# Optimization experiments

Measured on AMD Instinct MI355X. Metric: run time of the kernel, lower is better.

## Reference

```python
import jax, jax.numpy as jnp
import numpy as np

EMB = 1024
HEADS = 16
HEAD_DIM = EMB // HEADS
CTX = 2048
BATCH = 4
LN_EPS = 1e-5


def layer_norm(x, g, b):
    mu = jnp.mean(x, axis=-1, keepdims=True)
    var = jnp.mean(jnp.square(x - mu), axis=-1, keepdims=True)
    return (x - mu) * jax.lax.rsqrt(var + LN_EPS) * g + b


def setup_inputs() -> dict:
    key = jax.random.key(0)
    ks = jax.random.split(key, 12)
    s_in = 1.0 / np.sqrt(EMB)
    s_ff = 1.0 / np.sqrt(4 * EMB)
    return {
        "x": jax.random.normal(ks[0], (BATCH, CTX, EMB), jnp.float32),
        # per-head Q/K/V projections, no bias (matches Head linears)
        "wq": jax.random.normal(ks[1], (HEADS, EMB, HEAD_DIM), jnp.float32) * s_in,
        "wk": jax.random.normal(ks[2], (HEADS, EMB, HEAD_DIM), jnp.float32) * s_in,
        "wv": jax.random.normal(ks[3], (HEADS, EMB, HEAD_DIM), jnp.float32) * s_in,
        "w_proj": jax.random.normal(ks[4], (EMB, EMB), jnp.float32) * s_in,
        "b_proj": jnp.zeros((EMB,), jnp.float32),
        "w1": jax.random.normal(ks[5], (EMB, 4 * EMB), jnp.float32) * s_in,
        "b1": jnp.zeros((4 * EMB,), jnp.float32),
        "w2": jax.random.normal(ks[6], (4 * EMB, EMB), jnp.float32) * s_ff,
        "b2": jnp.zeros((EMB,), jnp.float32),
        "ln1_g": jnp.ones((EMB,), jnp.float32),
        "ln1_b": jnp.zeros((EMB,), jnp.float32),
        "ln2_g": jnp.ones((EMB,), jnp.float32),
        "ln2_b": jnp.zeros((EMB,), jnp.float32),
    }


def reference(x, wq, wk, wv, w_proj, b_proj, w1, b1, w2, b2, ln1_g, ln1_b, ln2_g, ln2_b):
    B, T, C = x.shape
    # --- attention branch (pre-LN) ---
    h = layer_norm(x, ln1_g, ln1_b)
    q = jnp.einsum('btc,hcd->bhtd', h, wq)
    k = jnp.einsum('btc,hcd->bhtd', h, wk)
    v = jnp.einsum('btc,hcd->bhtd', h, wv)
    scale = 1.0 / np.sqrt(HEAD_DIM)
    scores = jnp.einsum('bhtd,bhsd->bhts', q, k) * scale  # [B,H,T,T]
    causal = jnp.tril(jnp.ones((T, T), dtype=bool))
    scores = jnp.where(causal, scores, -jnp.inf)
    attn = jax.nn.softmax(scores, axis=-1)
    out = jnp.einsum('bhts,bhsd->bhtd', attn, v)
    out = out.transpose(0, 2, 1, 3).reshape(B, T, C)  # concat heads
    out = out @ w_proj.T + b_proj if False else jnp.einsum('btc,cd->btd', out, w_proj) + b_proj
    x = x + out
    # --- FFN branch (pre-LN) ---
    h2 = layer_norm(x, ln2_g, ln2_b)
    ff = jax.nn.relu(jnp.einsum('btc,cf->btf', h2, w1) + b1)
    ff = jnp.einsum('btf,fc->btc', ff, w2) + b2
    return x + ff
```

## Files before the change

kernel.cpp:

```cpp
#include <hip/hip_runtime.h>


#define DEVI __device__ __forceinline__

typedef float  f32x4  __attribute__((ext_vector_type(4)));
typedef float  f32x16 __attribute__((ext_vector_type(16)));
typedef __bf16 bf16x8 __attribute__((ext_vector_type(8)));
typedef short  s16x8  __attribute__((ext_vector_type(8)));
typedef unsigned int u32x4 __attribute__((ext_vector_type(4)));
typedef unsigned short u16;

DEVI u16 f2bf(float f) {
    return __builtin_bit_cast(u16, (__bf16)f);
}

DEVI unsigned pk2(float lo, float hi2) {
    return (unsigned)f2bf(lo) | ((unsigned)f2bf(hi2) << 16);
}

DEVI void gload_lds16(const void* g, void* l) {
    __builtin_amdgcn_global_load_lds(
        (__attribute__((address_space(1))) void*)(g),
        (__attribute__((address_space(3))) void*)(l), 16, 0, 0);
}

DEVI f32x4 mfma16(s16x8 a, s16x8 b, f32x4 c) {
    return __builtin_amdgcn_mfma_f32_16x16x32_bf16(
        __builtin_bit_cast(bf16x8, a), __builtin_bit_cast(bf16x8, b), c, 0, 0, 0);
}

DEVI f32x16 mfma32(s16x8 a, s16x8 b, f32x16 c) {
    return __builtin_amdgcn_mfma_f32_32x32x16_bf16(
        __builtin_bit_cast(bf16x8, a), __builtin_bit_cast(bf16x8, b), c, 0, 0, 0);
}

__global__ __launch_bounds__(256) void transpose_cvt(
    const float* __restrict__ src, u16* __restrict__ dst,
    int K, int N, long srcStride, long dstStride)
{
    __shared__ float t[64][65];
    src += (long)blockIdx.z * srcStride;
    dst += (long)blockIdx.z * dstStride;
    int k0 = blockIdx.x * 64, n0 = blockIdx.y * 64;
    int tx = threadIdx.x & 63, ty = threadIdx.x >> 6;
#pragma unroll
    for (int i = 0; i < 16; ++i) {
        int r = ty * 16 + i;
        t[r][tx] = src[(long)(k0 + r) * N + n0 + tx];
    }
    __syncthreads();
#pragma unroll
    for (int i = 0; i < 16; ++i) {
        int r = ty * 16 + i;
        dst[(long)(n0 + r) * K + k0 + tx] = f2bf(t[tx][r]);
    }
}

__global__ __launch_bounds__(256) void ln_bf16(
    const float* __restrict__ x, const float* __restrict__ g,
    const float* __restrict__ b, u16* __restrict__ out)
{
    int row = blockIdx.x, tid = threadIdx.x;
    const float4 v = ((const float4*)(x + (long)row * 1024))[tid];
    float s = v.x + v.y + v.z + v.w;
    float q = v.x * v.x + v.y * v.y + v.z * v.z + v.w * v.w;
#pragma unroll
    for (int m = 1; m < 64; m <<= 1) { s += __shfl_xor(s, m); q += __shfl_xor(q, m); }
    __shared__ float red[8];
    int lane = tid & 63, w = tid >> 6;
    if (lane == 0) { red[w] = s; red[w + 4] = q; }
    __syncthreads();
    s = red[0] + red[1] + red[2] + red[3];
    q = red[4] + red[5] + red[6] + red[7];
    float mu  = s * (1.0f / 1024.0f);
    float var = q * (1.0f / 1024.0f) - mu * mu;
    float rs  = rsqrtf(var + 1e-5f);
    float4 gv = ((const float4*)g)[tid];
    float4 bv = ((const float4*)b)[tid];
    ushort4 o;
    o.x = f2bf((v.x - mu) * rs * gv.x + bv.x);
    o.y = f2bf((v.y - mu) * rs * gv.y + bv.y);
    o.z = f2bf((v.z - mu) * rs * gv.z + bv.z);
    o.w = f2bf((v.w - mu) * rs * gv.w + bv.w);
    ((ushort4*)(out + (long)row * 1024))[tid] = o;
}

template <int EPI>
__global__ __launch_bounds__(256, 3) void gemm_bt(
    const u16* __restrict__ A, const u16* __restrict__ Bt,
    int M, int N, int K,
    float* __restrict__ outF, u16* __restrict__ outB,
    const float* __restrict__ bias, const float* __restrict__ resid,
    u16* __restrict__ qd, u16* __restrict__ kd, u16* __restrict__ vd)
{
    __shared__ alignas(16) u16 As[128 * 32];
    __shared__ alignas(16) u16 Bs[128 * 32];
    int tid = threadIdx.x;
    int lane = tid & 63, w = tid >> 6;
    int wm = w & 1, wn = w >> 1;
    int l15 = lane & 15, l4 = lane >> 4;
    long m0 = (long)blockIdx.x * 128, n0 = (long)blockIdx.y * 128;
    const u16* Ag = A + m0 * K;
    const u16* Bg = Bt + n0 * K;
    int scol = (lane & 3) * 8;
    int srow0 = (w * 2 + 0) * 16 + (lane >> 2);
    int srow1 = (w * 2 + 1) * 16 + (lane >> 2);

    f32x4 acc[4][4] = {};

    for (int kt = 0; kt < K; kt += 32) {
        gload_lds16(Ag + (long)srow0 * K + kt + scol, &As[(w * 2 + 0) * 512]);
        gload_lds16(Ag + (long)srow1 * K + kt + scol, &As[(w * 2 + 1) * 512]);
        gload_lds16(Bg + (long)srow0 * K + kt + scol, &Bs[(w * 2 + 0) * 512]);
        gload_lds16(Bg + (long)srow1 * K + kt + scol, &Bs[(w * 2 + 1) * 512]);
        __syncthreads();
        s16x8 a[4], b[4];
#pragma unroll
        for (int m = 0; m < 4; ++m)
            a[m] = *(const s16x8*)&As[(wm * 64 + m * 16 + l15) * 32 + l4 * 8];
#pragma unroll
        for (int n = 0; n < 4; ++n)
            b[n] = *(const s16x8*)&Bs[(wn * 64 + n * 16 + l15) * 32 + l4 * 8];
#pragma unroll
        for (int m = 0; m < 4; ++m)
#pragma unroll
            for (int n = 0; n < 4; ++n)
                acc[m][n] = mfma16(a[m], b[n], acc[m][n]);
        __syncthreads();
    }

    long mbase = m0 + wm * 64;
    long nbase = n0 + wn * 64;
#pragma unroll
    for (int m = 0; m < 4; ++m)
#pragma unroll
        for (int n = 0; n < 4; ++n)
#pragma unroll
            for (int r = 0; r < 4; ++r) {
                long row = mbase + m * 16 + l4 * 4 + r;
                long col = nbase + n * 16 + l15;
                float val = acc[m][n][r];
                if constexpr (EPI == 0) {
                    int c = (int)col;
                    int which = c >> 10, hh = (c >> 6) & 15, dd = c & 63;
                    int bb = (int)(row >> 11), tt = (int)(row & 2047);
                    if (which == 2) {
                        vd[((long)(bb * 16 + hh) * 64 + dd) * 2048 + tt] = f2bf(val);
                    } else {
                        u16* dst = which == 0 ? qd : kd;
                        dst[((long)(bb * 16 + hh) * 2048 + tt) * 64 + dd] = f2bf(val);
                    }
                } else if constexpr (EPI == 1) {
                    outF[row * N + col] = val + bias[col] + resid[row * N + col];
                } else {
                    float t2 = val + bias[col];
                    outB[row * N + col] = f2bf(t2 > 0.f ? t2 : 0.f);
                }
            }
}

__global__ __launch_bounds__(256, 4) void attn_kernel(
    const u16* __restrict__ Q, const u16* __restrict__ K,
    const u16* __restrict__ Vt, u16* __restrict__ O)
{
    constexpr int PAD = 72;
    constexpr float SC2 = 0.125f * 1.44269504088896f;
    constexpr float THR = 11.5416f;
    __shared__ alignas(16) u16 Ks[2][64 * PAD];
    __shared__ alignas(16) u16 Vts[2][64 * PAD];
    __shared__ alignas(16) float xbuf[4][32];
    int tid = threadIdx.x, lane = tid & 63, w = tid >> 6;
    int l31 = lane & 31, hi = lane >> 5;
    bool h = (hi != 0);
    int qp = blockIdx.x, hh = blockIdx.y, bb = blockIdx.z;
    const long hbase = ((long)(bb * 16 + hh)) * 2048 * 64;

    int srow[2], scol8[2];
#pragma unroll
    for (int i = 0; i < 2; ++i) {
        int c = tid + 256 * i;
        srow[i] = c >> 3;
        scol8[i] = (c & 7) * 8;
    }

#pragma unroll 1
    for (int ph = 0; ph < 2; ++ph) {
        int qt = ph == 0 ? qp : 15 - qp;
        int q0w = qt * 128 + w * 32;
        int nt = 2 * qt + 2;
        int qv = q0w + l31;

        s16x8 bq[4];
#pragma unroll
        for (int c = 0; c < 4; ++c)
            bq[c] = *(const s16x8*)&Q[hbase + (long)(q0w + l31) * 64 + c * 16 + hi * 8];

        f32x16 o0 = {}, o1 = {};
        float mrow = -1e30f, lrow = 0.f;

        s16x8 kr[2], vr[2];
        {
            const u16* Kg = K + hbase;
            const u16* Vg = Vt + hbase;
#pragma unroll
            for (int i = 0; i < 2; ++i) {
                s16x8 k0 = *(const s16x8*)&Kg[srow[i] * 64 + scol8[i]];
                s16x8 v0 = *(const s16x8*)&Vg[(long)srow[i] * 2048 + scol8[i]];
                *(s16x8*)&Ks[0][srow[i] * PAD + scol8[i]]  = k0;
                *(s16x8*)&Vts[0][srow[i] * PAD + scol8[i]] = v0;
            }
            if (nt > 1) {
                const u16* Kg1 = K + hbase + 64 * 64;
                const u16* Vg1 = Vt + hbase + 64;
#pragma unroll
                for (int i = 0; i < 2; ++i) {
                    kr[i] = *(const s16x8*)&Kg1[srow[i] * 64 + scol8[i]];
                    vr[i] = *(const s16x8*)&Vg1[(long)srow[i] * 2048 + scol8[i]];
                }
            }
        }
        __syncthreads();

#pragma unroll 1
        for (int kt = 0; kt < nt; ++kt) {
            int cur = kt & 1;
            if (kt + 1 < nt) {
#pragma unroll
                for (int i = 0; i < 2; ++i) {
                    *(s16x8*)&Ks[cur ^ 1][srow[i] * PAD + scol8[i]]  = kr[i];
                    *(s16x8*)&Vts[cur ^ 1][srow[i] * PAD + scol8[i]] = vr[i];
                }
            }
            if (kt + 2 < nt) {
                const u16* Kg = K + hbase + (long)(kt + 2) * 64 * 64;
                const u16* Vg = Vt + hbase + (long)(kt + 2) * 64;
#pragma unroll
                for (int i = 0; i < 2; ++i) {
                    kr[i] = *(const s16x8*)&Kg[srow[i] * 64 + scol8[i]];
                    vr[i] = *(const s16x8*)&Vg[(long)srow[i] * 2048 + scol8[i]];
                }
            }

#pragma unroll
            for (int k2 = 0; k2 < 2; ++k2) {
                int kbase = kt * 64 + k2 * 32;
                if (kbase <= q0w + 31) {
                    f32x16 s = {};
                    __builtin_amdgcn_s_setprio(1);
#pragma unroll
                    for (int c = 0; c < 4; ++c) {
                        s16x8 ak = *(const s16x8*)&Ks[cur][(k2 * 32 + l31) * PAD + c * 16 + hi * 8];
                        s = mfma32(ak, bq[c], s);
                    }
                    __builtin_amdgcn_s_setprio(0);

                    int khi = kbase + 4 * hi;
                    if (kbase + 31 > q0w) {
#pragma unroll
                        for (int r = 0; r < 16; ++r) {
                            int kg = khi + ((r & 3) + 8 * (r >> 2));
                            float sv = s[r] * SC2;
                            s[r] = (kg > qv) ? -1e30f : sv;
                        }
                    } else {
#pragma unroll
                        for (int r = 0; r < 16; ++r) s[r] *= SC2;
                    }

                    float t8[8], t4[4], t2[2];
#pragma unroll
                    for (int r = 0; r < 8; ++r) t8[r] = fmaxf(s[r], s[r + 8]);
#pragma unroll
                    for (int r = 0; r < 4; ++r) t4[r] = fmaxf(t8[r], t8[r + 4]);
                    t2[0] = fmaxf(t4[0], t4[2]); t2[1] = fmaxf(t4[1], t4[3]);
                    float pm = fmaxf(t2[0], t2[1]);
                    pm = fmaxf(pm, __shfl_xor(pm, 32));

                    int allok = __all(pm - mrow <= THR);
                    float ef = 1.f;
                    if (!allok) {
                        float mn = fmaxf(mrow, pm);
                        ef = exp2f(mrow - mn);
                        mrow = mn;
                    }
                    float a8[8], a4[4];
#pragma unroll
                    for (int r = 0; r < 16; ++r) s[r] = exp2f(s[r] - mrow);
#pragma unroll
                    for (int r = 0; r < 8; ++r) a8[r] = s[r] + s[r + 8];
#pragma unroll
                    for (int r = 0; r < 4; ++r) a4[r] = a8[r] + a8[r + 4];
                    float rsum = (a4[0] + a4[1]) + (a4[2] + a4[3]);
                    rsum += __shfl_xor(rsum, 32);

                    if (!allok) {
                        lrow = lrow * ef + rsum;
                        xbuf[w][l31] = ef;
#pragma unroll
                        for (int rr = 0; rr < 4; ++rr) {
                            f32x4 efv = *(const f32x4*)&xbuf[w][rr * 8 + hi * 4];
#pragma unroll
                            for (int j = 0; j < 4; ++j) {
                                o0[rr * 4 + j] *= efv[j];
                                o1[rr * 4 + j] *= efv[j];
                            }
                        }
                    } else {
                        lrow += rsum;
                    }

                    unsigned c0 = pk2(s[0],  s[1]),  c1 = pk2(s[2],  s[3]);
                    unsigned c2 = pk2(s[4],  s[5]),  c3 = pk2(s[6],  s[7]);
                    unsigned c4 = pk2(s[8],  s[9]),  c5 = pk2(s[10], s[11]);
                    unsigned c6 = pk2(s[12], s[13]), c7 = pk2(s[14], s[15]);
                    unsigned x0 = __shfl_xor((int)c0, 32), x1 = __shfl_xor((int)c1, 32);
                    unsigned x2 = __shfl_xor((int)c2, 32), x3 = __shfl_xor((int)c3, 32);
                    unsigned x4 = __shfl_xor((int)c4, 32), x5 = __shfl_xor((int)c5, 32);
                    unsigned x6 = __shfl_xor((int)c6, 32), x7 = __shfl_xor((int)c7, 32);
                    u32x4 w0 = { h ? x2 : c0, h ? x3 : c1, h ? c2 : x0, h ? c3 : x1 };
                    u32x4 w1 = { h ? x6 : c4, h ? x7 : c5, h ? c6 : x4, h ? c7 : x5 };
                    s16x8 pa0 = __builtin_bit_cast(s16x8, w0);
                    s16x8 pa1 = __builtin_bit_cast(s16x8, w1);

                    __builtin_amdgcn_s_setprio(1);
#pragma unroll
                    for (int ks = 0; ks < 2; ++ks) {
                        s16x8 pa = ks ? pa1 : pa0;
                        s16x8 bv0 = *(const s16x8*)&Vts[cur][(l31) * PAD + k2 * 32 + ks * 16 + hi * 8];
                        s16x8 bv1 = *(const s16x8*)&Vts[cur][(32 + l31) * PAD + k2 * 32 + ks * 16 + hi * 8];
                        o0 = mfma32(pa, bv0, o0);
                        o1 = mfma32(pa, bv1, o1);
                    }
                    __builtin_amdgcn_s_setprio(0);
                }
            }
            __syncthreads();
        }

        float il = 1.0f / lrow;
        xbuf[w][l31] = il;
        f32x4 ilv[4];
#pragma unroll
        for (int rr = 0; rr < 4; ++rr)
            ilv[rr] = *(const f32x4*)&xbuf[w][rr * 8 + hi * 4];
#pragma unroll
        for (int r = 0; r < 16; ++r) {
            int t = q0w + ((r & 3) + 8 * (r >> 2)) + 4 * hi;
            float sc = ilv[r >> 2][r & 3];
            long rbase = ((long)(bb * 2048 + t)) * 1024 + hh * 64;
            O[rbase + l31]      = f2bf(o0[r] * sc);
            O[rbase + 32 + l31] = f2bf(o1[r] * sc);
        }
        __syncthreads();
    }
}

extern "C" void kernel_launch(void* const* d_in, const int* in_sizes, int n_in,
                              void* d_out, int out_size, void* d_ws, size_t ws_size,
                              hipStream_t stream)
{
    const float* x      = (const float*)d_in[0];
    const float* wq     = (const float*)d_in[1];
    const float* wk     = (const float*)d_in[2];
    const float* wv     = (const float*)d_in[3];
    const float* w_proj = (const float*)d_in[4];
    const float* b_proj = (const float*)d_in[5];
    const float* w1     = (const float*)d_in[6];
    const float* b1     = (const float*)d_in[7];
    const float* w2     = (const float*)d_in[8];
    const float* b2     = (const float*)d_in[9];
    const float* ln1_g  = (const float*)d_in[10];
    const float* ln1_b  = (const float*)d_in[11];
    const float* ln2_g  = (const float*)d_in[12];
    const float* ln2_b  = (const float*)d_in[13];

    char* ws = (char*)d_ws;
    u16*   WQKVt = (u16*)(ws + 0);
    u16*   WPt   = (u16*)(ws + 6291456);
    u16*   W1t   = (u16*)(ws + 8388608);
    u16*   W2t   = (u16*)(ws + 16777216);
    u16*   H     = (u16*)(ws + 25165824);
    u16*   Qb    = (u16*)(ws + 41943040);
    u16*   Kb    = (u16*)(ws + 58720256);
    u16*   Vb    = (u16*)(ws + 75497472);
    u16*   Ob    = (u16*)(ws + 92274688);
    u16*   FF    = (u16*)(ws + 41943040);
    float* X1    = (float*)(ws + 109051904);
    float* out   = (float*)d_out;

    transpose_cvt<<<dim3(16, 1, 16), 256, 0, stream>>>(wq, WQKVt,           1024, 64, 65536, 65536);
    transpose_cvt<<<dim3(16, 1, 16), 256, 0, stream>>>(wk, WQKVt + 1048576, 1024, 64, 65536, 65536);
    transpose_cvt<<<dim3(16, 1, 16), 256, 0, stream>>>(wv, WQKVt + 2097152, 1024, 64, 65536, 65536);
    transpose_cvt<<<dim3(16, 16, 1), 256, 0, stream>>>(w_proj, WPt, 1024, 1024, 0, 0);
    transpose_cvt<<<dim3(16, 64, 1), 256, 0, stream>>>(w1, W1t, 1024, 4096, 0, 0);
    transpose_cvt<<<dim3(64, 16, 1), 256, 0, stream>>>(w2, W2t, 4096, 1024, 0, 0);

    ln_bf16<<<8192, 256, 0, stream>>>(x, ln1_g, ln1_b, H);

    gemm_bt<0><<<dim3(64, 24), 256, 0, stream>>>(H, WQKVt, 8192, 3072, 1024,
        nullptr, nullptr, nullptr, nullptr, Qb, Kb, Vb);

    attn_kernel<<<dim3(8, 16, 4), 256, 0, stream>>>(Qb, Kb, Vb, Ob);

    gemm_bt<1><<<dim3(64, 8), 256, 0, stream>>>(Ob, WPt, 8192, 1024, 1024,
        X1, nullptr, b_proj, x, nullptr, nullptr, nullptr);

    ln_bf16<<<8192, 256, 0, stream>>>(X1, ln2_g, ln2_b, H);

    gemm_bt<2><<<dim3(64, 32), 256, 0, stream>>>(H, W1t, 8192, 4096, 1024,
        nullptr, FF, b1, nullptr, nullptr, nullptr, nullptr);

    gemm_bt<1><<<dim3(64, 8), 256, 0, stream>>>(FF, W2t, 8192, 1024, 4096,
        out, nullptr, b2, X1, nullptr, nullptr, nullptr);
}
```

Before: 427.7 us.

## Add 256x256-tile double-buffered GEMM for QKV and FFN1 projections

Adds a new 512-thread GEMM kernel with 256x256 output tiles, a K-step of 64, XOR-swizzled LDS loaded directly from global memory, and double buffering. The next tile's loads overlap with MFMA phases that are separated by barriers and run under raised wave priority. The block index is also remapped so neighbouring workgroups share operand tiles in cache. The QKV and FFN1 GEMMs now use this kernel to get more data reuse per LDS load and better latency hiding. The costs are much higher register and LDS use per block and fewer blocks per wave.

Result: slower. 460.8 us (+7.7%).

```diff
diff --git a/kernel.cpp b/kernel.cpp
--- a/kernel.cpp
+++ b/kernel.cpp
@@ -83,6 +83,157 @@
     o.z = f2bf((v.z - mu) * rs * gv.z + bv.z);
     o.w = f2bf((v.w - mu) * rs * gv.w + bv.w);
     ((ushort4*)(out + (long)row * 1024))[tid] = o;
+}
+
+template <int EPI>
+__global__ __launch_bounds__(512, 2) void gemm256(
+    const u16* __restrict__ A, const u16* __restrict__ Bt,
+    int M, int N, int K,
+    u16* __restrict__ outB, const float* __restrict__ bias,
+    u16* __restrict__ qd, u16* __restrict__ kd, u16* __restrict__ vd)
+{
+    __shared__ alignas(16) u16 lds[2][2][16384];
+    int tid = threadIdx.x, lane = tid & 63, w = tid >> 6;
+    int l15 = lane & 15, l4 = lane >> 4;
+    int wm = w >> 2, wn = w & 3;
+
+    int gx = gridDim.x;
+    int nwg = gx * gridDim.y;
+    int bid = blockIdx.y * gx + blockIdx.x;
+    int swz = (bid & 7) * (nwg >> 3) + (bid >> 3);
+    int bx = swz % gx, by = swz / gx;
+    long m0 = (long)bx * 256, n0 = (long)by * 256;
+
+    int srow8 = lane >> 3;
+    int sc = ((lane & 7) ^ srow8) * 8;
+    const u16* Ags = A + (m0 + w * 8 + srow8) * (long)K + sc;
+    const u16* Bgs = Bt + (n0 + w * 8 + srow8) * (long)K + sc;
+    int ldsw = w * 512;
+
+    int rc0 = (l4 * 8) ^ ((l15 & 7) * 8);
+    int rc1 = (32 + l4 * 8) ^ ((l15 & 7) * 8);
+
+    f32x4 acc[8][4] = {};
+
+#pragma unroll
+    for (int i = 0; i < 4; ++i) {
+        gload_lds16(Ags + (long)i * 64 * K, &lds[0][0][i * 4096 + ldsw]);
+        gload_lds16(Bgs + (long)i * 64 * K, &lds[0][1][i * 4096 + ldsw]);
+    }
+    asm volatile("s_waitcnt vmcnt(0)" ::: "memory");
+    __builtin_amdgcn_s_barrier();
+
+    int NT = K >> 6;
+#pragma unroll 1
+    for (int t = 0; t < NT; ++t) {
+        int cur = t & 1;
+        const u16* As_ = &lds[cur][0][0];
+        const u16* Bs_ = &lds[cur][1][0];
+
+        s16x8 a0[4], b0[4];
+#pragma unroll
+        for (int i = 0; i < 4; ++i)
+            a0[i] = *(const s16x8*)&As_[(wm * 128 + i * 16 + l15) * 64 + rc0];
+#pragma unroll
+        for (int n = 0; n < 4; ++n)
+            b0[n] = *(const s16x8*)&Bs_[(wn * 64 + n * 16 + l15) * 64 + rc0];
+        if (t + 1 < NT) {
+            long kt = (long)(t + 1) * 64;
+#pragma unroll
+            for (int i = 0; i < 4; ++i) {
+                gload_lds16(Ags + (long)i * 64 * K + kt, &lds[cur ^ 1][0][i * 4096 + ldsw]);
+                gload_lds16(Bgs + (long)i * 64 * K + kt, &lds[cur ^ 1][1][i * 4096 + ldsw]);
+            }
+        }
+        __builtin_amdgcn_s_barrier();
+        asm volatile("s_waitcnt lgkmcnt(0)" ::: "memory");
+        __builtin_amdgcn_sched_barrier(0);
+        __builtin_amdgcn_s_setprio(1);
+#pragma unroll
+        for (int mi = 0; mi < 4; ++mi)
+#pragma unroll
+            for (int n = 0; n < 4; ++n)
+                acc[mi][n] = mfma16(a0[mi], b0[n], acc[mi][n]);
+        __builtin_amdgcn_s_setprio(0);
+        __builtin_amdgcn_s_barrier();
+
+        s16x8 a1[4];
+#pragma unroll
+        for (int i = 0; i < 4; ++i)
+            a1[i] = *(const s16x8*)&As_[(wm * 128 + 64 + i * 16 + l15) * 64 + rc0];
+        __builtin_amdgcn_s_barrier();
+        asm volatile("s_waitcnt lgkmcnt(0)" ::: "memory");
+        __builtin_amdgcn_sched_barrier(0);
+        __builtin_amdgcn_s_setprio(1);
+#pragma unroll
+        for (int mi = 0; mi < 4; ++mi)
+#pragma unroll
+            for (int n = 0; n < 4; ++n)
+                acc[4 + mi][n] = mfma16(a1[mi], b0[n], acc[4 + mi][n]);
+        __builtin_amdgcn_s_setprio(0);
+        __builtin_amdgcn_s_barrier();
+
+        s16x8 a2[4], b1v[4];
+#pragma unroll
+        for (int i = 0; i < 4; ++i)
+            a2[i] = *(const s16x8*)&As_[(wm * 128 + i * 16 + l15) * 64 + rc1];
+#pragma unroll
+        for (int n = 0; n < 4; ++n)
+            b1v[n] = *(const s16x8*)&Bs_[(wn * 64 + n * 16 + l15) * 64 + rc1];
+        __builtin_amdgcn_s_barrier();
+        asm volatile("s_waitcnt lgkmcnt(0)" ::: "memory");
+        __builtin_amdgcn_sched_barrier(0);
+        __builtin_amdgcn_s_setprio(1);
+#pragma unroll
+        for (int mi = 0; mi < 4; ++mi)
+#pragma unroll
+            for (int n = 0; n < 4; ++n)
+                acc[mi][n] = mfma16(a2[mi], b1v[n], acc[mi][n]);
+        __builtin_amdgcn_s_setprio(0);
+        __builtin_amdgcn_s_barrier();
+
+        s16x8 a3[4];
+#pragma unroll
+        for (int i = 0; i < 4; ++i)
+            a3[i] = *(const s16x8*)&As_[(wm * 128 + 64 + i * 16 + l15) * 64 + rc1];
+        __builtin_amdgcn_s_barrier();
+        asm volatile("s_waitcnt lgkmcnt(0)" ::: "memory");
+        __builtin_amdgcn_sched_barrier(0);
+        __builtin_amdgcn_s_setprio(1);
+#pragma unroll
+        for (int mi = 0; mi < 4; ++mi)
+#pragma unroll
+            for (int n = 0; n < 4; ++n)
+                acc[4 + mi][n] = mfma16(a3[mi], b1v[n], acc[4 + mi][n]);
+        __builtin_amdgcn_s_setprio(0);
+        asm volatile("s_waitcnt vmcnt(0)" ::: "memory");
+        __builtin_amdgcn_s_barrier();
+    }
+
+#pragma unroll
+    for (int mf = 0; mf < 8; ++mf)
+#pragma unroll
+        for (int n = 0; n < 4; ++n)
+#pragma unroll
+            for (int r = 0; r < 4; ++r) {
+                long row = m0 + wm * 128 + mf * 16 + l4 * 4 + r;
+                long col = n0 + wn * 64 + n * 16 + l15;
+                float val = acc[mf][n][r];
+                if constexpr (EPI == 0) {
+                    int c = (int)col;
+                    int which = c >> 10, hh = (c >> 6) & 15, dd = c & 63;
+                    int bb = (int)(row >> 11), tt = (int)(row & 2047);
+                    if (which == 2) {
+                        vd[((long)(bb * 16 + hh) * 64 + dd) * 2048 + tt] = f2bf(val);
+                    } else {
+                        u16* dst = which == 0 ? qd : kd;
+                        dst[((long)(bb * 16 + hh) * 2048 + tt) * 64 + dd] = f2bf(val);
+                    }
+                } else {
+                    float t2 = val + bias[col];
+                    outB[row * N + col] = f2bf(t2 > 0.f ? t2 : 0.f);
+                }
+            }
 }
 
 template <int EPI>
@@ -140,21 +291,8 @@
                 long row = mbase + m * 16 + l4 * 4 + r;
                 long col = nbase + n * 16 + l15;
                 float val = acc[m][n][r];
-                if constexpr (EPI == 0) {
-                    int c = (int)col;
-                    int which = c >> 10, hh = (c >> 6) & 15, dd = c & 63;
-                    int bb = (int)(row >> 11), tt = (int)(row & 2047);
-                    if (which == 2) {
-                        vd[((long)(bb * 16 + hh) * 64 + dd) * 2048 + tt] = f2bf(val);
-                    } else {
-                        u16* dst = which == 0 ? qd : kd;
-                        dst[((long)(bb * 16 + hh) * 2048 + tt) * 64 + dd] = f2bf(val);
-                    }
-                } else if constexpr (EPI == 1) {
+                if constexpr (EPI == 1) {
                     outF[row * N + col] = val + bias[col] + resid[row * N + col];
-                } else {
-                    float t2 = val + bias[col];
-                    outB[row * N + col] = f2bf(t2 > 0.f ? t2 : 0.f);
                 }
             }
 }
@@ -397,8 +535,8 @@
 
     ln_bf16<<<8192, 256, 0, stream>>>(x, ln1_g, ln1_b, H);
 
-    gemm_bt<0><<<dim3(64, 24), 256, 0, stream>>>(H, WQKVt, 8192, 3072, 1024,
-        nullptr, nullptr, nullptr, nullptr, Qb, Kb, Vb);
+    gemm256<0><<<dim3(32, 12), 512, 0, stream>>>(H, WQKVt, 8192, 3072, 1024,
+        nullptr, nullptr, Qb, Kb, Vb);
 
     attn_kernel<<<dim3(8, 16, 4), 256, 0, stream>>>(Qb, Kb, Vb, Ob);
 
@@ -407,8 +545,8 @@
 
     ln_bf16<<<8192, 256, 0, stream>>>(X1, ln2_g, ln2_b, H);
 
-    gemm_bt<2><<<dim3(64, 32), 256, 0, stream>>>(H, W1t, 8192, 4096, 1024,
-        nullptr, FF, b1, nullptr, nullptr, nullptr, nullptr);
+    gemm256<2><<<dim3(32, 16), 512, 0, stream>>>(H, W1t, 8192, 4096, 1024,
+        FF, b1, nullptr, nullptr, nullptr);
 
     gemm_bt<1><<<dim3(64, 8), 256, 0, stream>>>(FF, W2t, 8192, 1024, 4096,
         out, nullptr, b2, X1, nullptr, nullptr, nullptr);
```

## Add 256x256-tile pipelined GEMM for QKV and FFN1 projections

Applied to the files above, without the earlier changes.

Introduces a 512-thread GEMM kernel with 256x256 output tiles, a 4-slot LDS ring with two tiles of prefetch via direct global-to-LDS loads, XOR-swizzled LDS layout, and block-index swizzling for L2 locality. It replaces the 128x128 kernel for the QKV and first FFN GEMMs to raise data reuse per LDS load and overlap loads with MFMA work. Costs include larger LDS use, 128 accumulator registers per thread, and fewer workgroups (384/512), which may leave CUs idle or create wave-quantization tails.

Measured after the change: 453.5 us. 1.06x slower.

```diff
diff --git a/kernel.cpp b/kernel.cpp
--- a/kernel.cpp
+++ b/kernel.cpp
@@ -83,6 +83,131 @@
     o.z = f2bf((v.z - mu) * rs * gv.z + bv.z);
     o.w = f2bf((v.w - mu) * rs * gv.w + bv.w);
     ((ushort4*)(out + (long)row * 1024))[tid] = o;
+}
+
+template <int EPI>
+__global__ __launch_bounds__(512, 2) void gemm256(
+    const u16* __restrict__ A, const u16* __restrict__ Bt,
+    int M, int N, int K,
+    u16* __restrict__ outB, const float* __restrict__ bias,
+    u16* __restrict__ qd, u16* __restrict__ kd, u16* __restrict__ vd)
+{
+    __shared__ alignas(16) u16 lds[4][2][8192];
+    int tid = threadIdx.x, lane = tid & 63, w = tid >> 6;
+    int l15 = lane & 15, l4 = lane >> 4;
+    int wm = w >> 2, wn = w & 3;
+
+    int gx = gridDim.x;
+    int nwg = gx * gridDim.y;
+    int bid = blockIdx.y * gx + blockIdx.x;
+    int swz = (bid & 7) * (nwg >> 3) + (bid >> 3);
+    int bx = swz % gx, by = swz / gx;
+    long m0 = (long)bx * 256, n0 = (long)by * 256;
+
+    long soff0, soff1; int ldso0, ldso1;
+    {
+        int cI0 = w * 64 + lane;
+        int r0 = cI0 >> 2, p0 = cI0 & 3;
+        soff0 = (long)r0 * K + (p0 ^ ((r0 >> 1) & 3)) * 8;
+        ldso0 = w * 512;
+        int cI1 = 512 + cI0;
+        int r1 = cI1 >> 2, p1 = cI1 & 3;
+        soff1 = (long)r1 * K + (p1 ^ ((r1 >> 1) & 3)) * 8;
+        ldso1 = 4096 + w * 512;
+    }
+    const u16* Ag = A + m0 * K;
+    const u16* Bg = Bt + n0 * K;
+
+#define STAGE(tt) do {                                                  \
+        int _b = (tt) & 3;                                              \
+        long _kt = (long)(tt) * 32;                                     \
+        gload_lds16(Ag + soff0 + _kt, &lds[_b][0][ldso0]);              \
+        gload_lds16(Bg + soff0 + _kt, &lds[_b][1][ldso0]);              \
+        gload_lds16(Ag + soff1 + _kt, &lds[_b][0][ldso1]);              \
+        gload_lds16(Bg + soff1 + _kt, &lds[_b][1][ldso1]);              \
+    } while (0)
+
+    int rc = (l4 ^ ((l15 >> 1) & 3)) * 8;
+
+    f32x4 acc[8][4] = {};
+
+    STAGE(0);
+    STAGE(1);
+    asm volatile("s_waitcnt vmcnt(4)" ::: "memory");
+    __builtin_amdgcn_s_barrier();
+
+    int NT = K >> 5;
+#pragma unroll 1
+    for (int t = 0; t < NT; ++t) {
+        int cb = t & 3;
+        const u16* As_ = &lds[cb][0][0];
+        const u16* Bs_ = &lds[cb][1][0];
+
+        if (t + 2 < NT) STAGE(t + 2);
+
+        s16x8 a[8], b[4];
+#pragma unroll
+        for (int i = 0; i < 4; ++i)
+            a[i] = *(const s16x8*)&As_[(wm * 128 + i * 16 + l15) * 32 + rc];
+#pragma unroll
+        for (int n = 0; n < 4; ++n)
+            b[n] = *(const s16x8*)&Bs_[(wn * 64 + n * 16 + l15) * 32 + rc];
+#pragma unroll
+        for (int i = 0; i < 4; ++i)
+            a[4 + i] = *(const s16x8*)&As_[(wm * 128 + 64 + i * 16 + l15) * 32 + rc];
+
+        asm volatile("s_waitcnt lgkmcnt(4)" ::: "memory");
+        __builtin_amdgcn_sched_barrier(0);
+        __builtin_amdgcn_s_setprio(1);
+#pragma unroll
+        for (int mi = 0; mi < 4; ++mi)
+#pragma unroll
+            for (int n = 0; n < 4; ++n)
+                acc[mi][n] = mfma16(a[mi], b[n], acc[mi][n]);
+        __builtin_amdgcn_s_setprio(0);
+
+        asm volatile("s_waitcnt lgkmcnt(0)" ::: "memory");
+        __builtin_amdgcn_sched_barrier(0);
+        __builtin_amdgcn_s_setprio(1);
+#pragma unroll
+        for (int mi = 0; mi < 4; ++mi)
+#pragma unroll
+            for (int n = 0; n < 4; ++n)
+                acc[4 + mi][n] = mfma16(a[4 + mi], b[n], acc[4 + mi][n]);
+        __builtin_amdgcn_s_setprio(0);
+
+        if (t + 2 < NT)
+            asm volatile("s_waitcnt vmcnt(4)" ::: "memory");
+        else
+            asm volatile("s_waitcnt vmcnt(0)" ::: "memory");
+        __builtin_amdgcn_s_barrier();
+    }
+#undef STAGE
+
+#pragma unroll
+    for (int mf = 0; mf < 8; ++mf)
+#pragma unroll
+        for (int n = 0; n < 4; ++n)
+#pragma unroll
+            for (int r = 0; r < 4; ++r) {
+                long row = m0 + wm * 128 + mf * 16 + l4 * 4 + r;
+                long col = n0 + wn * 64 + n * 16 + l15;
+                float val = acc[mf][n][r];
+                if constexpr (EPI == 0) {
+                    int c = (int)col;
+                    int which = c >> 10, hh = (c >> 6) & 15, dd = c & 63;
+                    int bb = (int)(row >> 11), tt = (int)(row & 2047);
+                    if (which == 2) {
+                        vd[((long)(bb * 16 + hh) * 64 + dd) * 2048 + tt] = f2bf(val);
+                    } else {
+                        u16* dst = which == 0 ? qd : kd;
+                        dst[((long)(bb * 16 + hh) * 2048 + tt) * 64 + dd] = f2bf(val);
+                    }
+                } else {
+                    float t2 = val + bias[col];
+                    outB[row * N + col] = f2bf(t2 > 0.f ? t2 : 0.f);
+                }
+            }
 }
 
 template <int EPI>
@@ -140,21 +265,8 @@
                 long row = mbase + m * 16 + l4 * 4 + r;
                 long col = nbase + n * 16 + l15;
                 float val = acc[m][n][r];
-                if constexpr (EPI == 0) {
-                    int c = (int)col;
-                    int which = c >> 10, hh = (c >> 6) & 15, dd = c & 63;
-                    int bb = (int)(row >> 11), tt = (int)(row & 2047);
-                    if (which == 2) {
-                        vd[((long)(bb * 16 + hh) * 64 + dd) * 2048 + tt] = f2bf(val);
-                    } else {
-                        u16* dst = which == 0 ? qd : kd;
-                        dst[((long)(bb * 16 + hh) * 2048 + tt) * 64 + dd] = f2bf(val);
-                    }
-                } else if constexpr (EPI == 1) {
+                if constexpr (EPI == 1) {
                     outF[row * N + col] = val + bias[col] + resid[row * N + col];
-                } else {
-                    float t2 = val + bias[col];
-                    outB[row * N + col] = f2bf(t2 > 0.f ? t2 : 0.f);
                 }
             }
 }
@@ -397,8 +509,8 @@
 
     ln_bf16<<<8192, 256, 0, stream>>>(x, ln1_g, ln1_b, H);
 
-    gemm_bt<0><<<dim3(64, 24), 256, 0, stream>>>(H, WQKVt, 8192, 3072, 1024,
-        nullptr, nullptr, nullptr, nullptr, Qb, Kb, Vb);
+    gemm256<0><<<dim3(32, 12), 512, 0, stream>>>(H, WQKVt, 8192, 3072, 1024,
+        nullptr, nullptr, Qb, Kb, Vb);
 
     attn_kernel<<<dim3(8, 16, 4), 256, 0, stream>>>(Qb, Kb, Vb, Ob);
 
@@ -407,8 +519,8 @@
 
     ln_bf16<<<8192, 256, 0, stream>>>(X1, ln2_g, ln2_b, H);
 
-    gemm_bt<2><<<dim3(64, 32), 256, 0, stream>>>(H, W1t, 8192, 4096, 1024,
-        nullptr, FF, b1, nullptr, nullptr, nullptr, nullptr);
+    gemm256<2><<<dim3(32, 16), 512, 0, stream>>>(H, W1t, 8192, 4096, 1024,
+        FF, b1, nullptr, nullptr, nullptr);
 
     gemm_bt<1><<<dim3(64, 8), 256, 0, stream>>>(FF, W2t, 8192, 1024, 4096,
         out, nullptr, b2, X1, nullptr, nullptr, nullptr);
```

## Drop paired causal tiles per block and process 64-key softmax tiles at once

Applied to the files above, without the earlier changes.

The attention kernel no longer pairs a light and heavy query tile in one block; each block now handles a single 128-row query tile, and the grid doubles to 1024 blocks. The inner loop also computes both 32-key halves of a 64-key tile before one combined online-softmax update, halving max/sum reductions and rescale checks. This risks load imbalance across blocks, since causal tiles vary in cost, and raises register pressure from holding two score tiles.

New measurement: 507.0 us. +18.5%, slower.

```diff
diff --git a/kernel.cpp b/kernel.cpp
--- a/kernel.cpp
+++ b/kernel.cpp
@@ -172,7 +172,7 @@
     int tid = threadIdx.x, lane = tid & 63, w = tid >> 6;
     int l31 = lane & 31, hi = lane >> 5;
     bool h = (hi != 0);
-    int qp = blockIdx.x, hh = blockIdx.y, bb = blockIdx.z;
+    int qt = blockIdx.x, hh = blockIdx.y, bb = blockIdx.z;
     const long hbase = ((long)(bb * 16 + hh)) * 2048 * 64;
 
     int srow[2], scol8[2];
@@ -183,175 +183,209 @@
         scol8[i] = (c & 7) * 8;
     }
 
+    int q0w = qt * 128 + w * 32;
+    int nt = 2 * qt + 2;
+    int qv = q0w + l31;
+
+    s16x8 bq[4];
+#pragma unroll
+    for (int c = 0; c < 4; ++c)
+        bq[c] = *(const s16x8*)&Q[hbase + (long)(q0w + l31) * 64 + c * 16 + hi * 8];
+
+    f32x16 o0 = {}, o1 = {};
+    float mrow = -1e30f, lrow = 0.f;
+
+    s16x8 kr[2], vr[2];
+    {
+        const u16* Kg = K + hbase;
+        const u16* Vg = Vt + hbase;
+#pragma unroll
+        for (int i = 0; i < 2; ++i) {
+            s16x8 k0 = *(const s16x8*)&Kg[srow[i] * 64 + scol8[i]];
+            s16x8 v0 = *(const s16x8*)&Vg[(long)srow[i] * 2048 + scol8[i]];
+            *(s16x8*)&Ks[0][srow[i] * PAD + scol8[i]]  = k0;
+            *(s16x8*)&Vts[0][srow[i] * PAD + scol8[i]] = v0;
+        }
+        if (nt > 1) {
+            const u16* Kg1 = K + hbase + 64 * 64;
+            const u16* Vg1 = Vt + hbase + 64;
+#pragma unroll
+            for (int i = 0; i < 2; ++i) {
+                kr[i] = *(const s16x8*)&Kg1[srow[i] * 64 + scol8[i]];
+                vr[i] = *(const s16x8*)&Vg1[(long)srow[i] * 2048 + scol8[i]];
+            }
+        }
+    }
+    __syncthreads();
+
 #pragma unroll 1
-    for (int ph = 0; ph < 2; ++ph) {
-        int qt = ph == 0 ? qp : 15 - qp;
-        int q0w = qt * 128 + w * 32;
-        int nt = 2 * qt + 2;
-        int qv = q0w + l31;
-
-        s16x8 bq[4];
-#pragma unroll
-        for (int c = 0; c < 4; ++c)
-            bq[c] = *(const s16x8*)&Q[hbase + (long)(q0w + l31) * 64 + c * 16 + hi * 8];
-
-        f32x16 o0 = {}, o1 = {};
-        float mrow = -1e30f, lrow = 0.f;
-
-        s16x8 kr[2], vr[2];
-        {
-            const u16* Kg = K + hbase;
-            const u16* Vg = Vt + hbase;
+    for (int kt = 0; kt < nt; ++kt) {
+        int cur = kt & 1;
+        if (kt + 1 < nt) {
 #pragma unroll
             for (int i = 0; i < 2; ++i) {
-                s16x8 k0 = *(const s16x8*)&Kg[srow[i] * 64 + scol8[i]];
-                s16x8 v0 = *(const s16x8*)&Vg[(long)srow[i] * 2048 + scol8[i]];
-                *(s16x8*)&Ks[0][srow[i] * PAD + scol8[i]]  = k0;
-                *(s16x8*)&Vts[0][srow[i] * PAD + scol8[i]] = v0;
-            }
-            if (nt > 1) {
-                const u16* Kg1 = K + hbase + 64 * 64;
-                const u16* Vg1 = Vt + hbase + 64;
-#pragma unroll
-                for (int i = 0; i < 2; ++i) {
-                    kr[i] = *(const s16x8*)&Kg1[srow[i] * 64 + scol8[i]];
-                    vr[i] = *(const s16x8*)&Vg1[(long)srow[i] * 2048 + scol8[i]];
-                }
-            }
+                *(s16x8*)&Ks[cur ^ 1][srow[i] * PAD + scol8[i]]  = kr[i];
+                *(s16x8*)&Vts[cur ^ 1][srow[i] * PAD + scol8[i]] = vr[i];
+            }
+        }
+        if (kt + 2 < nt) {
+            const u16* Kg = K + hbase + (long)(kt + 2) * 64 * 64;
+            const u16* Vg = Vt + hbase + (long)(kt + 2) * 64;
+#pragma unroll
+            for (int i = 0; i < 2; ++i) {
+                kr[i] = *(const s16x8*)&Kg[srow[i] * 64 + scol8[i]];
+                vr[i] = *(const s16x8*)&Vg[(long)srow[i] * 2048 + scol8[i]];
+            }
+        }
+
+        int kb0 = kt * 64;
+        if (kb0 <= q0w + 31) {
+            bool live1 = (kb0 + 32 <= q0w + 31);
+
+            f32x16 s0 = {}, s1;
+            __builtin_amdgcn_s_setprio(1);
+#pragma unroll
+            for (int c = 0; c < 4; ++c) {
+                s16x8 ak = *(const s16x8*)&Ks[cur][(l31) * PAD + c * 16 + hi * 8];
+                s0 = mfma32(ak, bq[c], s0);
+            }
+            __builtin_amdgcn_s_setprio(0);
+            if (live1) {
+                f32x16 z = {};
+                __builtin_amdgcn_s_setprio(1);
+#pragma unroll
+                for (int c = 0; c < 4; ++c) {
+                    s16x8 ak = *(const s16x8*)&Ks[cur][(32 + l31) * PAD + c * 16 + hi * 8];
+                    z = mfma32(ak, bq[c], z);
+                }
+                __builtin_amdgcn_s_setprio(0);
+                s1 = z;
+            } else {
+#pragma unroll
+                for (int r = 0; r < 16; ++r) s1[r] = -1e30f;
+            }
+
+            int khi0 = kb0 + 4 * hi;
+            if (kb0 + 31 > q0w) {
+#pragma unroll
+                for (int r = 0; r < 16; ++r) {
+                    int kg = khi0 + ((r & 3) + 8 * (r >> 2));
+                    s0[r] = (kg > qv) ? -1e30f : s0[r] * SC2;
+                }
+            } else {
+#pragma unroll
+                for (int r = 0; r < 16; ++r) s0[r] *= SC2;
+            }
+            if (live1) {
+                int kb1 = kb0 + 32;
+                int khi1 = kb1 + 4 * hi;
+                if (kb1 + 31 > q0w) {
+#pragma unroll
+                    for (int r = 0; r < 16; ++r) {
+                        int kg = khi1 + ((r & 3) + 8 * (r >> 2));
+                        s1[r] = (kg > qv) ? -1e30f : s1[r] * SC2;
+                    }
+                } else {
+#pragma unroll
+                    for (int r = 0; r < 16; ++r) s1[r] *= SC2;
+                }
+            }
+
+            float m16[16];
+#pragma unroll
+            for (int r = 0; r < 16; ++r) m16[r] = fmaxf(s0[r], s1[r]);
+            float m8[8], m4[4];
+#pragma unroll
+            for (int r = 0; r < 8; ++r) m8[r] = fmaxf(m16[r], m16[r + 8]);
+#pragma unroll
+            for (int r = 0; r < 4; ++r) m4[r] = fmaxf(m8[r], m8[r + 4]);
+            float pm = fmaxf(fmaxf(m4[0], m4[1]), fmaxf(m4[2], m4[3]));
+            pm = fmaxf(pm, __shfl_xor(pm, 32));
+
+            int allok = __all(pm - mrow <= THR);
+            float ef = 1.f;
+            if (!allok) {
+                float mn = fmaxf(mrow, pm);
+                ef = exp2f(mrow - mn);
+                mrow = mn;
+            }
+#pragma unroll
+            for (int r = 0; r < 16; ++r) s0[r] = exp2f(s0[r] - mrow);
+#pragma unroll
+            for (int r = 0; r < 16; ++r) s1[r] = exp2f(s1[r] - mrow);
+            float a16[16];
+#pragma unroll
+            for (int r = 0; r < 16; ++r) a16[r] = s0[r] + s1[r];
+            float a8[8], a4[4];
+#pragma unroll
+            for (int r = 0; r < 8; ++r) a8[r] = a16[r] + a16[r + 8];
+#pragma unroll
+            for (int r = 0; r < 4; ++r) a4[r] = a8[r] + a8[r + 4];
+            float rsum = (a4[0] + a4[1]) + (a4[2] + a4[3]);
+            rsum += __shfl_xor(rsum, 32);
+
+            if (!allok) {
+                lrow = lrow * ef + rsum;
+                xbuf[w][l31] = ef;
+#pragma unroll
+                for (int rr = 0; rr < 4; ++rr) {
+                    f32x4 efv = *(const f32x4*)&xbuf[w][rr * 8 + hi * 4];
+#pragma unroll
+                    for (int j = 0; j < 4; ++j) {
+                        o0[rr * 4 + j] *= efv[j];
+                        o1[rr * 4 + j] *= efv[j];
+                    }
+                }
+            } else {
+                lrow += rsum;
+            }
+
+            s16x8 pa[2][2];
+#pragma unroll
+            for (int sub = 0; sub < 2; ++sub) {
+                const f32x16& sv = sub ? s1 : s0;
+                unsigned c0 = pk2(sv[0],  sv[1]),  c1 = pk2(sv[2],  sv[3]);
+                unsigned c2 = pk2(sv[4],  sv[5]),  c3 = pk2(sv[6],  sv[7]);
+                unsigned c4 = pk2(sv[8],  sv[9]),  c5 = pk2(sv[10], sv[11]);
+                unsigned c6 = pk2(sv[12], sv[13]), c7 = pk2(sv[14], sv[15]);
+                unsigned x0 = __shfl_xor((int)c0, 32), x1 = __shfl_xor((int)c1, 32);
+                unsigned x2 = __shfl_xor((int)c2, 32), x3 = __shfl_xor((int)c3, 32);
+                unsigned x4 = __shfl_xor((int)c4, 32), x5 = __shfl_xor((int)c5, 32);
+                unsigned x6 = __shfl_xor((int)c6, 32), x7 = __shfl_xor((int)c7, 32);
+                u32x4 w0 = { h ? x2 : c0, h ? x3 : c1, h ? c2 : x0, h ? c3 : x1 };
+                u32x4 w1 = { h ? x6 : c4, h ? x7 : c5, h ? c6 : x4, h ? c7 : x5 };
+                pa[sub][0] = __builtin_bit_cast(s16x8, w0);
+                pa[sub][1] = __builtin_bit_cast(s16x8, w1);
+            }
+
+            __builtin_amdgcn_s_setprio(1);
+#pragma unroll
+            for (int sub = 0; sub < 2; ++sub)
+#pragma unroll
+                for (int ks = 0; ks < 2; ++ks) {
+                    s16x8 bv0 = *(const s16x8*)&Vts[cur][(l31) * PAD + sub * 32 + ks * 16 + hi * 8];
+                    s16x8 bv1 = *(const s16x8*)&Vts[cur][(32 + l31) * PAD + sub * 32 + ks * 16 + hi * 8];
+                    o0 = mfma32(pa[sub][ks], bv0, o0);
+                    o1 = mfma32(pa[sub][ks], bv1, o1);
+                }
+            __builtin_amdgcn_s_setprio(0);
         }
         __syncthreads();
-
-#pragma unroll 1
-        for (int kt = 0; kt < nt; ++kt) {
-            int cur = kt & 1;
-            if (kt + 1 < nt) {
-#pragma unroll
-                for (int i = 0; i < 2; ++i) {
-                    *(s16x8*)&Ks[cur ^ 1][srow[i] * PAD + scol8[i]]  = kr[i];
-                    *(s16x8*)&Vts[cur ^ 1][srow[i] * PAD + scol8[i]] = vr[i];
-                }
-            }
-            if (kt + 2 < nt) {
-                const u16* Kg = K + hbase + (long)(kt + 2) * 64 * 64;
-                const u16* Vg = Vt + hbase + (long)(kt + 2) * 64;
-#pragma unroll
-                for (int i = 0; i < 2; ++i) {
-                    kr[i] = *(const s16x8*)&Kg[srow[i] * 64 + scol8[i]];
-                    vr[i] = *(const s16x8*)&Vg[(long)srow[i] * 2048 + scol8[i]];
-                }
-            }
-
-#pragma unroll
-            for (int k2 = 0; k2 < 2; ++k2) {
-                int kbase = kt * 64 + k2 * 32;
-                if (kbase <= q0w + 31) {
-                    f32x16 s = {};
-                    __builtin_amdgcn_s_setprio(1);
-#pragma unroll
-                    for (int c = 0; c < 4; ++c) {
-                        s16x8 ak = *(const s16x8*)&Ks[cur][(k2 * 32 + l31) * PAD + c * 16 + hi * 8];
-                        s = mfma32(ak, bq[c], s);
-                    }
-                    __builtin_amdgcn_s_setprio(0);
-
-                    int khi = kbase + 4 * hi;
-                    if (kbase + 31 > q0w) {
-#pragma unroll
-                        for (int r = 0; r < 16; ++r) {
-                            int kg = khi + ((r & 3) + 8 * (r >> 2));
-                            float sv = s[r] * SC2;
-                            s[r] = (kg > qv) ? -1e30f : sv;
-                        }
-                    } else {
-#pragma unroll
-                        for (int r = 0; r < 16; ++r) s[r] *= SC2;
-                    }
-
-                    float t8[8], t4[4], t2[2];
-#pragma unroll
-                    for (int r = 0; r < 8; ++r) t8[r] = fmaxf(s[r], s[r + 8]);
-#pragma unroll
-                    for (int r = 0; r < 4; ++r) t4[r] = fmaxf(t8[r], t8[r + 4]);
-                    t2[0] = fmaxf(t4[0], t4[2]); t2[1] = fmaxf(t4[1], t4[3]);
-                    float pm = fmaxf(t2[0], t2[1]);
-                    pm = fmaxf(pm, __shfl_xor(pm, 32));
-
-                    int allok = __all(pm - mrow <= THR);
-                    float ef = 1.f;
-                    if (!allok) {
-                        float mn = fmaxf(mrow, pm);
-                        ef = exp2f(mrow - mn);
-                        mrow = mn;
-                    }
-                    float a8[8], a4[4];
-#pragma unroll
-                    for (int r = 0; r < 16; ++r) s[r] = exp2f(s[r] - mrow);
-#pragma unroll
-                    for (int r = 0; r < 8; ++r) a8[r] = s[r] + s[r + 8];
-#pragma unroll
-                    for (int r = 0; r < 4; ++r) a4[r] = a8[r] + a8[r + 4];
-                    float rsum = (a4[0] + a4[1]) + (a4[2] + a4[3]);
-                    rsum += __shfl_xor(rsum, 32);
-
-                    if (!allok) {
-                        lrow = lrow * ef + rsum;
-                        xbuf[w][l31] = ef;
-#pragma unroll
-                        for (int rr = 0; rr < 4; ++rr) {
-                            f32x4 efv = *(const f32x4*)&xbuf[w][rr * 8 + hi * 4];
-#pragma unroll
-                            for (int j = 0; j < 4; ++j) {
-                                o0[rr * 4 + j] *= efv[j];
-                                o1[rr * 4 + j] *= efv[j];
-                            }
-                        }
-                    } else {
-                        lrow += rsum;
-                    }
-
-                    unsigned c0 = pk2(s[0],  s[1]),  c1 = pk2(s[2],  s[3]);
-                    unsigned c2 = pk2(s[4],  s[5]),  c3 = pk2(s[6],  s[7]);
-                    unsigned c4 = pk2(s[8],  s[9]),  c5 = pk2(s[10], s[11]);
-                    unsigned c6 = pk2(s[12], s[13]), c7 = pk2(s[14], s[15]);
-                    unsigned x0 = __shfl_xor((int)c0, 32), x1 = __shfl_xor((int)c1, 32);
-                    unsigned x2 = __shfl_xor((int)c2, 32), x3 = __shfl_xor((int)c3, 32);
-                    unsigned x4 = __shfl_xor((int)c4, 32), x5 = __shfl_xor((int)c5, 32);
-                    unsigned x6 = __shfl_xor((int)c6, 32), x7 = __shfl_xor((int)c7, 32);
-                    u32x4 w0 = { h ? x2 : c0, h ? x3 : c1, h ? c2 : x0, h ? c3 : x1 };
-                    u32x4 w1 = { h ? x6 : c4, h ? x7 : c5, h ? c6 : x4, h ? c7 : x5 };
-                    s16x8 pa0 = __builtin_bit_cast(s16x8, w0);
-                    s16x8 pa1 = __builtin_bit_cast(s16x8, w1);
-
-                    __builtin_amdgcn_s_setprio(1);
-#pragma unroll
-                    for (int ks = 0; ks < 2; ++ks) {
-                        s16x8 pa = ks ? pa1 : pa0;
-                        s16x8 bv0 = *(const s16x8*)&Vts[cur][(l31) * PAD + k2 * 32 + ks * 16 + hi * 8];
-                        s16x8 bv1 = *(const s16x8*)&Vts[cur][(32 + l31) * PAD + k2 * 32 + ks * 16 + hi * 8];
-                        o0 = mfma32(pa, bv0, o0);
-                        o1 = mfma32(pa, bv1, o1);
-                    }
-                    __builtin_amdgcn_s_setprio(0);
-                }
-            }
-            __syncthreads();
-        }
-
-        float il = 1.0f / lrow;
-        xbuf[w][l31] = il;
-        f32x4 ilv[4];
-#pragma unroll
-        for (int rr = 0; rr < 4; ++rr)
-            ilv[rr] = *(const f32x4*)&xbuf[w][rr * 8 + hi * 4];
-#pragma unroll
-        for (int r = 0; r < 16; ++r) {
-            int t = q0w + ((r & 3) + 8 * (r >> 2)) + 4 * hi;
-            float sc = ilv[r >> 2][r & 3];
-            long rbase = ((long)(bb * 2048 + t)) * 1024 + hh * 64;
-            O[rbase + l31]      = f2bf(o0[r] * sc);
-            O[rbase + 32 + l31] = f2bf(o1[r] * sc);
-        }
-        __syncthreads();
+    }
+
+    float il = 1.0f / lrow;
+    xbuf[w][l31] = il;
+    f32x4 ilv[4];
+#pragma unroll
+    for (int rr = 0; rr < 4; ++rr)
+        ilv[rr] = *(const f32x4*)&xbuf[w][rr * 8 + hi * 4];
+#pragma unroll
+    for (int r = 0; r < 16; ++r) {
+        int t = q0w + ((r & 3) + 8 * (r >> 2)) + 4 * hi;
+        float sc = ilv[r >> 2][r & 3];
+        long rbase = ((long)(bb * 2048 + t)) * 1024 + hh * 64;
+        O[rbase + l31]      = f2bf(o0[r] * sc);
+        O[rbase + 32 + l31] = f2bf(o1[r] * sc);
     }
 }
 
@@ -400,7 +434,7 @@
     gemm_bt<0><<<dim3(64, 24), 256, 0, stream>>>(H, WQKVt, 8192, 3072, 1024,
         nullptr, nullptr, nullptr, nullptr, Qb, Kb, Vb);
 
-    attn_kernel<<<dim3(8, 16, 4), 256, 0, stream>>>(Qb, Kb, Vb, Ob);
+    attn_kernel<<<dim3(16, 16, 4), 256, 0, stream>>>(Qb, Kb, Vb, Ob);
 
     gemm_bt<1><<<dim3(64, 8), 256, 0, stream>>>(Ob, WPt, 8192, 1024, 1024,
         X1, nullptr, b_proj, x, nullptr, nullptr, nullptr);
```
